# Performance work log

Measured on AMD Instinct MI355X. Metric: run time of the kernel, lower is better.

Reference implementation:

```python
import jax, jax.numpy as jnp
import numpy as np
import math

B, L, H, E = 4, 2048, 8, 64


def setup_inputs() -> dict:
    key = jax.random.key(0)
    kq, kk, kv, ks = jax.random.split(key, 4)
    return {
        "queries": jax.random.normal(kq, (B, L, H, E), dtype=jnp.float32),
        "keys": jax.random.normal(kk, (B, L, H, E), dtype=jnp.float32),
        "values": jax.random.normal(kv, (B, L, H, E), dtype=jnp.float32),
        "sigma": jax.random.normal(ks, (B, L, H), dtype=jnp.float32),
    }


def reference(queries, keys, values, sigma):
    Bq, Lq, Hq, Eq = queries.shape
    scale = 1.0 / math.sqrt(Eq)
    # QK^T: [B, H, L, S]
    scores = jnp.einsum("blhe,bshe->bhls", queries, keys)
    # triangular causal mask (mask_flag=True, attn_mask=None)
    causal = jnp.triu(jnp.ones((Lq, Lq), dtype=bool), k=1)
    scores = jnp.where(causal[None, None], -jnp.inf, scores)
    attn = scale * scores
    series = jax.nn.softmax(attn, axis=-1)  # dropout p=0.0 -> identity
    # sigma: [B, L, H] -> [B, H, L]
    sig = jnp.transpose(sigma, (0, 2, 1))
    sig = jax.nn.sigmoid(sig * 5.0) + 1e-5
    sig = jnp.power(3.0, sig) - 1.0
    sig = jnp.broadcast_to(sig[..., None], (Bq, Hq, Lq, Lq))  # [B,H,L,L]
    # |i - j| distances
    idx = jnp.arange(Lq, dtype=jnp.float32)
    dist = jnp.abs(idx[:, None] - idx[None, :])  # [L, L]
    prior = (1.0 / (math.sqrt(2.0 * math.pi) * sig)) * jnp.exp(
        -(dist[None, None] ** 2) / (2.0 * sig ** 2)
    )
    V = jnp.einsum("bhls,bshd->blhd", series, values)
    return V, series, prior, sig
```

## Files before the change

### kernel.cpp

```cpp
#include <hip/hip_runtime.h>
#include <math.h>

#define BB 4
#define LL 2048
#define HH 8
#define EE 64
#define TM 64
#define TN 64

static constexpr float SCALE = 0.125f;
static constexpr float LN3 = 1.0986122886681098f;
static constexpr float INV_SQRT_2PI = 0.3989422804014327f;
static constexpr size_t NMAT = (size_t)BB * HH * LL * LL;
static constexpr size_t SERIES_BASE = (size_t)BB * LL * HH * EE;
static constexpr size_t PRIOR_BASE = SERIES_BASE + NMAT;
static constexpr size_t SIG_BASE = PRIOR_BASE + NMAT;

__device__ __forceinline__ float dot4(float4 a, float4 b) {
  return a.x * b.x + a.y * b.y + a.z * b.z + a.w * b.w;
}
__device__ __forceinline__ void fma4(float4& acc, float s, float4 v) {
  acc.x += s * v.x; acc.y += s * v.y; acc.z += s * v.z; acc.w += s * v.w;
}

__global__ __launch_bounds__(256, 3)
void anomaly_attn(const float* __restrict__ qg,
                  const float* __restrict__ kg,
                  const float* __restrict__ vg,
                  const float* __restrict__ sgg,
                  float* __restrict__ out) {
  __shared__ float4 Qs[TM][17];
  __shared__ float4 KPs[TN][17];
  __shared__ float4 Vs[TN][17];
  __shared__ float s_linv[TM];
  __shared__ float s_sigv[TM], s_pinv[TM], s_c2[TM];

  const int t = threadIdx.x;
  const int bh = blockIdx.y;
  const int b = bh >> 3;
  const int h = bh & 7;
  const int tx = t & 15;
  const int ty = t >> 4;

  const float4* q4 = (const float4*)qg;
  const float4* k4 = (const float4*)kg;
  const float4* v4 = (const float4*)vg;
  float* Pf = (float*)&KPs[0][0];

  for (int half = 0; half < 2; ++half) {
    const int rt = (half == 0) ? (int)blockIdx.x : (LL / TM - 1 - (int)blockIdx.x);
    const int i0 = rt * TM;
    const int nt = rt + 1;

    __syncthreads();

    for (int idx = t; idx < TM * 16; idx += 256) {
      int r = idx >> 4, c = idx & 15;
      Qs[r][c] = q4[(((size_t)b * LL + (i0 + r)) * HH + h) * 16 + c];
    }
    if (t < TM) {
      float sg = sgg[((size_t)b * LL + (i0 + t)) * HH + h];
      float sd = 1.0f / (1.0f + __expf(-5.0f * sg)) + 1e-5f;
      float sv = expm1f(sd * LN3);
      s_sigv[t] = sv;
      s_pinv[t] = INV_SQRT_2PI / sv;
      s_c2[t] = 0.5f / (sv * sv);
    }

    float lr0 = 0.f, lr1 = 0.f, lr2 = 0.f, lr3 = 0.f;
    for (int jt = 0; jt < nt; ++jt) {
      const int j0 = jt * TN;
      __syncthreads();
      for (int idx = t; idx < TN * 16; idx += 256) {
        int r = idx >> 4, c = idx & 15;
        KPs[r][c] = k4[(((size_t)b * LL + (j0 + r)) * HH + h) * 16 + c];
      }
      __syncthreads();
      float S[4][4] = {};
      for (int e4 = 0; e4 < 16; ++e4) {
        float4 qv0 = Qs[ty][e4];
        float4 qv1 = Qs[ty + 16][e4];
        float4 qv2 = Qs[ty + 32][e4];
        float4 qv3 = Qs[ty + 48][e4];
        float4 kv0 = KPs[tx][e4];
        float4 kv1 = KPs[tx + 16][e4];
        float4 kv2 = KPs[tx + 32][e4];
        float4 kv3 = KPs[tx + 48][e4];
        S[0][0] += dot4(qv0, kv0); S[0][1] += dot4(qv0, kv1);
        S[0][2] += dot4(qv0, kv2); S[0][3] += dot4(qv0, kv3);
        S[1][0] += dot4(qv1, kv0); S[1][1] += dot4(qv1, kv1);
        S[1][2] += dot4(qv1, kv2); S[1][3] += dot4(qv1, kv3);
        S[2][0] += dot4(qv2, kv0); S[2][1] += dot4(qv2, kv1);
        S[2][2] += dot4(qv2, kv2); S[2][3] += dot4(qv2, kv3);
        S[3][0] += dot4(qv3, kv0); S[3][1] += dot4(qv3, kv1);
        S[3][2] += dot4(qv3, kv2); S[3][3] += dot4(qv3, kv3);
      }
#pragma unroll
      for (int cc = 0; cc < 4; ++cc) {
        int j = j0 + tx + 16 * cc;
        lr0 += (j <= i0 + ty)      ? __expf(S[0][cc] * SCALE) : 0.f;
        lr1 += (j <= i0 + ty + 16) ? __expf(S[1][cc] * SCALE) : 0.f;
        lr2 += (j <= i0 + ty + 32) ? __expf(S[2][cc] * SCALE) : 0.f;
        lr3 += (j <= i0 + ty + 48) ? __expf(S[3][cc] * SCALE) : 0.f;
      }
    }
#pragma unroll
    for (int m = 1; m < 16; m <<= 1) {
      lr0 += __shfl_xor(lr0, m);
      lr1 += __shfl_xor(lr1, m);
      lr2 += __shfl_xor(lr2, m);
      lr3 += __shfl_xor(lr3, m);
    }
    if (tx == 0) {
      s_linv[ty] = 1.0f / lr0;
      s_linv[ty + 16] = 1.0f / lr1;
      s_linv[ty + 32] = 1.0f / lr2;
      s_linv[ty + 48] = 1.0f / lr3;
    }
    __syncthreads();

    const float li0 = s_linv[ty];
    const float li1 = s_linv[ty + 16];
    const float li2 = s_linv[ty + 32];
    const float li3 = s_linv[ty + 48];
    float4 acc0 = {0, 0, 0, 0}, acc1 = {0, 0, 0, 0};
    float4 acc2 = {0, 0, 0, 0}, acc3 = {0, 0, 0, 0};
    for (int jt = 0; jt < nt; ++jt) {
      const int j0 = jt * TN;
      __syncthreads();
      for (int idx = t; idx < TN * 16; idx += 256) {
        int r = idx >> 4, c = idx & 15;
        size_t g = (((size_t)b * LL + (j0 + r)) * HH + h) * 16 + c;
        KPs[r][c] = k4[g];
        Vs[r][c] = v4[g];
      }
      __syncthreads();
      float S[4][4] = {};
      for (int e4 = 0; e4 < 16; ++e4) {
        float4 qv0 = Qs[ty][e4];
        float4 qv1 = Qs[ty + 16][e4];
        float4 qv2 = Qs[ty + 32][e4];
        float4 qv3 = Qs[ty + 48][e4];
        float4 kv0 = KPs[tx][e4];
        float4 kv1 = KPs[tx + 16][e4];
        float4 kv2 = KPs[tx + 32][e4];
        float4 kv3 = KPs[tx + 48][e4];
        S[0][0] += dot4(qv0, kv0); S[0][1] += dot4(qv0, kv1);
        S[0][2] += dot4(qv0, kv2); S[0][3] += dot4(qv0, kv3);
        S[1][0] += dot4(qv1, kv0); S[1][1] += dot4(qv1, kv1);
        S[1][2] += dot4(qv1, kv2); S[1][3] += dot4(qv1, kv3);
        S[2][0] += dot4(qv2, kv0); S[2][1] += dot4(qv2, kv1);
        S[2][2] += dot4(qv2, kv2); S[2][3] += dot4(qv2, kv3);
        S[3][0] += dot4(qv3, kv0); S[3][1] += dot4(qv3, kv1);
        S[3][2] += dot4(qv3, kv2); S[3][3] += dot4(qv3, kv3);
      }
      __syncthreads();
#pragma unroll
      for (int cc = 0; cc < 4; ++cc) {
        int j = j0 + tx + 16 * cc;
        int col = tx + 16 * cc;
        Pf[(ty) * 68 + col]      = (j <= i0 + ty)      ? __expf(S[0][cc] * SCALE) * li0 : 0.f;
        Pf[(ty + 16) * 68 + col] = (j <= i0 + ty + 16) ? __expf(S[1][cc] * SCALE) * li1 : 0.f;
        Pf[(ty + 32) * 68 + col] = (j <= i0 + ty + 32) ? __expf(S[2][cc] * SCALE) * li2 : 0.f;
        Pf[(ty + 48) * 68 + col] = (j <= i0 + ty + 48) ? __expf(S[3][cc] * SCALE) * li3 : 0.f;
      }
      __syncthreads();
#pragma unroll
      for (int m = 0; m < 4; ++m) {
        int idx = t + 256 * m;
        int rr = idx >> 4, jq = idx & 15;
        float4 pv = KPs[rr][jq];
        *(float4*)&out[SERIES_BASE + ((size_t)bh * LL + (i0 + rr)) * LL + j0 + jq * 4] = pv;
      }
#pragma unroll 4
      for (int j4 = 0; j4 < 16; ++j4) {
        float4 p0 = KPs[ty][j4];
        float4 p1 = KPs[ty + 16][j4];
        float4 p2 = KPs[ty + 32][j4];
        float4 p3 = KPs[ty + 48][j4];
        float4 va = Vs[j4 * 4 + 0][tx];
        float4 vb = Vs[j4 * 4 + 1][tx];
        float4 vc = Vs[j4 * 4 + 2][tx];
        float4 vd = Vs[j4 * 4 + 3][tx];
        fma4(acc0, p0.x, va); fma4(acc0, p0.y, vb); fma4(acc0, p0.z, vc); fma4(acc0, p0.w, vd);
        fma4(acc1, p1.x, va); fma4(acc1, p1.y, vb); fma4(acc1, p1.z, vc); fma4(acc1, p1.w, vd);
        fma4(acc2, p2.x, va); fma4(acc2, p2.y, vb); fma4(acc2, p2.z, vc); fma4(acc2, p2.w, vd);
        fma4(acc3, p3.x, va); fma4(acc3, p3.y, vb); fma4(acc3, p3.z, vc); fma4(acc3, p3.w, vd);
      }
    }
    {
      float4* o4 = (float4*)out;
      o4[(((size_t)b * LL + (i0 + ty)) * HH + h) * 16 + tx] = acc0;
      o4[(((size_t)b * LL + (i0 + ty + 16)) * HH + h) * 16 + tx] = acc1;
      o4[(((size_t)b * LL + (i0 + ty + 32)) * HH + h) * 16 + tx] = acc2;
      o4[(((size_t)b * LL + (i0 + ty + 48)) * HH + h) * 16 + tx] = acc3;
    }
    for (int idx = t; idx < TM * 512; idx += 256) {
      int rr = idx >> 9, jq = idx & 511;
      float iv = s_pinv[rr], c2 = s_c2[rr], sv = s_sigv[rr];
      float fi = (float)(i0 + rr);
      float d0 = fi - (float)(jq * 4);
      float d1 = d0 - 1.0f, d2 = d0 - 2.0f, d3 = d0 - 3.0f;
      float4 pr;
      pr.x = iv * __expf(-d0 * d0 * c2);
      pr.y = iv * __expf(-d1 * d1 * c2);
      pr.z = iv * __expf(-d2 * d2 * c2);
      pr.w = iv * __expf(-d3 * d3 * c2);
      size_t off = ((size_t)bh * LL + (i0 + rr)) * LL + jq * 4;
      *(float4*)&out[PRIOR_BASE + off] = pr;
      float4 sg4 = {sv, sv, sv, sv};
      *(float4*)&out[SIG_BASE + off] = sg4;
    }
    {
      int jz = nt * TN;
      int nz4 = (LL - jz) >> 2;
      if (nz4 > 0) {
        float4 z = {0, 0, 0, 0};
        for (int rr = 0; rr < TM; ++rr) {
          float* rowp = &out[SERIES_BASE + ((size_t)bh * LL + (i0 + rr)) * LL + jz];
          for (int c = t; c < nz4; c += 256) {
            *(float4*)&rowp[c * 4] = z;
          }
        }
      }
    }
  }
}

extern "C" void kernel_launch(void* const* d_in, const int* in_sizes, int n_in,
                              void* d_out, int out_size, void* d_ws, size_t ws_size,
                              hipStream_t stream) {
  const float* q = (const float*)d_in[0];
  const float* k = (const float*)d_in[1];
  const float* v = (const float*)d_in[2];
  const float* sg = (const float*)d_in[3];
  float* out = (float*)d_out;
  dim3 grid(LL / TM / 2, BB * HH);
  anomaly_attn<<<grid, 256, 0, stream>>>(q, k, v, sg, out);
}
```

Before: 2.015 ms.

## Use fp16 MFMA for QK^T and PV matmuls in anomaly attention

Replaces the scalar fp32 dot-product loops for QK^T and P·V with 16x16x32 fp16 MFMA instructions. Q, K and a transposed V are converted to half precision in shared memory, and the normalized probabilities are stored as fp16 and reused both for the series output and as the MFMA A operand. The per-row sum reduction now stays in registers instead of going through shared memory. The output tensor is dominated by large L×L writes (series, prior, sigma), so compute savings may matter less than memory traffic. Series values lose precision because they are rounded to fp16 before being written, and occupancy bounds drop from 3 to 2 blocks.

Result: faster. 1.711 ms (-15.1%).

```diff
diff --git a/kernel.cpp b/kernel.cpp
--- a/kernel.cpp
+++ b/kernel.cpp
@@ -7,6 +7,11 @@
 #define EE 64
 #define TM 64
 #define TN 64
+#define SH 72
+
+typedef _Float16 half4v __attribute__((ext_vector_type(4)));
+typedef _Float16 half8v __attribute__((ext_vector_type(8)));
+typedef float floatx4 __attribute__((ext_vector_type(4)));
 
 static constexpr float SCALE = 0.125f;
 static constexpr float LN3 = 1.0986122886681098f;
@@ -16,47 +21,42 @@
 static constexpr size_t PRIOR_BASE = SERIES_BASE + NMAT;
 static constexpr size_t SIG_BASE = PRIOR_BASE + NMAT;
 
-__device__ __forceinline__ float dot4(float4 a, float4 b) {
-  return a.x * b.x + a.y * b.y + a.z * b.z + a.w * b.w;
-}
-__device__ __forceinline__ void fma4(float4& acc, float s, float4 v) {
-  acc.x += s * v.x; acc.y += s * v.y; acc.z += s * v.z; acc.w += s * v.w;
-}
-
-__global__ __launch_bounds__(256, 3)
+__global__ __launch_bounds__(256, 2)
 void anomaly_attn(const float* __restrict__ qg,
                   const float* __restrict__ kg,
                   const float* __restrict__ vg,
                   const float* __restrict__ sgg,
                   float* __restrict__ out) {
-  __shared__ float4 Qs[TM][17];
-  __shared__ float4 KPs[TN][17];
-  __shared__ float4 Vs[TN][17];
-  __shared__ float s_linv[TM];
+  __shared__ __attribute__((aligned(16))) _Float16 Qh[TM * SH];
+  __shared__ __attribute__((aligned(16))) _Float16 Kh[TN * SH];
+  __shared__ __attribute__((aligned(16))) _Float16 Vt[EE * SH];
+  __shared__ __attribute__((aligned(16))) _Float16 Ph[TM * SH];
   __shared__ float s_sigv[TM], s_pinv[TM], s_c2[TM];
 
   const int t = threadIdx.x;
+  const int lane = t & 63;
+  const int w = t >> 6;
+  const int quad = lane >> 4;
+  const int l15 = lane & 15;
   const int bh = blockIdx.y;
-  const int b = bh >> 3;
-  const int h = bh & 7;
-  const int tx = t & 15;
-  const int ty = t >> 4;
-
+  const int b = bh >> 3, h = bh & 7;
   const float4* q4 = (const float4*)qg;
   const float4* k4 = (const float4*)kg;
   const float4* v4 = (const float4*)vg;
-  float* Pf = (float*)&KPs[0][0];
 
   for (int half = 0; half < 2; ++half) {
-    const int rt = (half == 0) ? (int)blockIdx.x : (LL / TM - 1 - (int)blockIdx.x);
+    const int rt = half ? (31 - (int)blockIdx.x) : (int)blockIdx.x;
     const int i0 = rt * TM;
     const int nt = rt + 1;
-
     __syncthreads();
 
-    for (int idx = t; idx < TM * 16; idx += 256) {
+#pragma unroll
+    for (int it = 0; it < 4; ++it) {
+      int idx = t + 256 * it;
       int r = idx >> 4, c = idx & 15;
-      Qs[r][c] = q4[(((size_t)b * LL + (i0 + r)) * HH + h) * 16 + c];
+      float4 qv = q4[(((size_t)b * LL + i0 + r) * HH + h) * 16 + c];
+      half4v hq = {(_Float16)qv.x, (_Float16)qv.y, (_Float16)qv.z, (_Float16)qv.w};
+      *(half4v*)&Qh[r * SH + c * 4] = hq;
     }
     if (t < TM) {
       float sg = sgg[((size_t)b * LL + (i0 + t)) * HH + h];
@@ -67,133 +67,132 @@
       s_c2[t] = 0.5f / (sv * sv);
     }
 
-    float lr0 = 0.f, lr1 = 0.f, lr2 = 0.f, lr3 = 0.f;
+    float lsum[4] = {0.f, 0.f, 0.f, 0.f};
     for (int jt = 0; jt < nt; ++jt) {
       const int j0 = jt * TN;
       __syncthreads();
-      for (int idx = t; idx < TN * 16; idx += 256) {
+#pragma unroll
+      for (int it = 0; it < 4; ++it) {
+        int idx = t + 256 * it;
         int r = idx >> 4, c = idx & 15;
-        KPs[r][c] = k4[(((size_t)b * LL + (j0 + r)) * HH + h) * 16 + c];
-      }
-      __syncthreads();
-      float S[4][4] = {};
-      for (int e4 = 0; e4 < 16; ++e4) {
-        float4 qv0 = Qs[ty][e4];
-        float4 qv1 = Qs[ty + 16][e4];
-        float4 qv2 = Qs[ty + 32][e4];
-        float4 qv3 = Qs[ty + 48][e4];
-        float4 kv0 = KPs[tx][e4];
-        float4 kv1 = KPs[tx + 16][e4];
-        float4 kv2 = KPs[tx + 32][e4];
-        float4 kv3 = KPs[tx + 48][e4];
-        S[0][0] += dot4(qv0, kv0); S[0][1] += dot4(qv0, kv1);
-        S[0][2] += dot4(qv0, kv2); S[0][3] += dot4(qv0, kv3);
-        S[1][0] += dot4(qv1, kv0); S[1][1] += dot4(qv1, kv1);
-        S[1][2] += dot4(qv1, kv2); S[1][3] += dot4(qv1, kv3);
-        S[2][0] += dot4(qv2, kv0); S[2][1] += dot4(qv2, kv1);
-        S[2][2] += dot4(qv2, kv2); S[2][3] += dot4(qv2, kv3);
-        S[3][0] += dot4(qv3, kv0); S[3][1] += dot4(qv3, kv1);
-        S[3][2] += dot4(qv3, kv2); S[3][3] += dot4(qv3, kv3);
-      }
-#pragma unroll
-      for (int cc = 0; cc < 4; ++cc) {
-        int j = j0 + tx + 16 * cc;
-        lr0 += (j <= i0 + ty)      ? __expf(S[0][cc] * SCALE) : 0.f;
-        lr1 += (j <= i0 + ty + 16) ? __expf(S[1][cc] * SCALE) : 0.f;
-        lr2 += (j <= i0 + ty + 32) ? __expf(S[2][cc] * SCALE) : 0.f;
-        lr3 += (j <= i0 + ty + 48) ? __expf(S[3][cc] * SCALE) : 0.f;
-      }
-    }
-#pragma unroll
-    for (int m = 1; m < 16; m <<= 1) {
-      lr0 += __shfl_xor(lr0, m);
-      lr1 += __shfl_xor(lr1, m);
-      lr2 += __shfl_xor(lr2, m);
-      lr3 += __shfl_xor(lr3, m);
-    }
-    if (tx == 0) {
-      s_linv[ty] = 1.0f / lr0;
-      s_linv[ty + 16] = 1.0f / lr1;
-      s_linv[ty + 32] = 1.0f / lr2;
-      s_linv[ty + 48] = 1.0f / lr3;
-    }
-    __syncthreads();
-
-    const float li0 = s_linv[ty];
-    const float li1 = s_linv[ty + 16];
-    const float li2 = s_linv[ty + 32];
-    const float li3 = s_linv[ty + 48];
-    float4 acc0 = {0, 0, 0, 0}, acc1 = {0, 0, 0, 0};
-    float4 acc2 = {0, 0, 0, 0}, acc3 = {0, 0, 0, 0};
+        float4 kv = k4[(((size_t)b * LL + j0 + r) * HH + h) * 16 + c];
+        half4v hk = {(_Float16)kv.x, (_Float16)kv.y, (_Float16)kv.z, (_Float16)kv.w};
+        *(half4v*)&Kh[r * SH + c * 4] = hk;
+      }
+      __syncthreads();
+      floatx4 acc[4] = {{0.f, 0.f, 0.f, 0.f}, {0.f, 0.f, 0.f, 0.f},
+                        {0.f, 0.f, 0.f, 0.f}, {0.f, 0.f, 0.f, 0.f}};
+#pragma unroll
+      for (int ks = 0; ks < 2; ++ks) {
+        half8v a = *(half8v*)&Qh[(w * 16 + l15) * SH + ks * 32 + quad * 8];
+#pragma unroll
+        for (int f = 0; f < 4; ++f) {
+          half8v bf = *(half8v*)&Kh[(f * 16 + l15) * SH + ks * 32 + quad * 8];
+          acc[f] = __builtin_amdgcn_mfma_f32_16x16x32_f16(a, bf, acc[f], 0, 0, 0);
+        }
+      }
+#pragma unroll
+      for (int f = 0; f < 4; ++f) {
+        int j = j0 + f * 16 + l15;
+#pragma unroll
+        for (int r = 0; r < 4; ++r) {
+          int i = i0 + w * 16 + quad * 4 + r;
+          lsum[r] += (j <= i) ? __expf(acc[f][r] * SCALE) : 0.f;
+        }
+      }
+    }
+#pragma unroll
+    for (int r = 0; r < 4; ++r) {
+      lsum[r] += __shfl_xor(lsum[r], 1);
+      lsum[r] += __shfl_xor(lsum[r], 2);
+      lsum[r] += __shfl_xor(lsum[r], 4);
+      lsum[r] += __shfl_xor(lsum[r], 8);
+    }
+    float linv[4];
+#pragma unroll
+    for (int r = 0; r < 4; ++r) linv[r] = 1.0f / lsum[r];
+
+    floatx4 Oacc[4] = {{0.f, 0.f, 0.f, 0.f}, {0.f, 0.f, 0.f, 0.f},
+                       {0.f, 0.f, 0.f, 0.f}, {0.f, 0.f, 0.f, 0.f}};
     for (int jt = 0; jt < nt; ++jt) {
       const int j0 = jt * TN;
       __syncthreads();
-      for (int idx = t; idx < TN * 16; idx += 256) {
+#pragma unroll
+      for (int it = 0; it < 4; ++it) {
+        int idx = t + 256 * it;
         int r = idx >> 4, c = idx & 15;
-        size_t g = (((size_t)b * LL + (j0 + r)) * HH + h) * 16 + c;
-        KPs[r][c] = k4[g];
-        Vs[r][c] = v4[g];
-      }
-      __syncthreads();
-      float S[4][4] = {};
-      for (int e4 = 0; e4 < 16; ++e4) {
-        float4 qv0 = Qs[ty][e4];
-        float4 qv1 = Qs[ty + 16][e4];
-        float4 qv2 = Qs[ty + 32][e4];
-        float4 qv3 = Qs[ty + 48][e4];
-        float4 kv0 = KPs[tx][e4];
-        float4 kv1 = KPs[tx + 16][e4];
-        float4 kv2 = KPs[tx + 32][e4];
-        float4 kv3 = KPs[tx + 48][e4];
-        S[0][0] += dot4(qv0, kv0); S[0][1] += dot4(qv0, kv1);
-        S[0][2] += dot4(qv0, kv2); S[0][3] += dot4(qv0, kv3);
-        S[1][0] += dot4(qv1, kv0); S[1][1] += dot4(qv1, kv1);
-        S[1][2] += dot4(qv1, kv2); S[1][3] += dot4(qv1, kv3);
-        S[2][0] += dot4(qv2, kv0); S[2][1] += dot4(qv2, kv1);
-        S[2][2] += dot4(qv2, kv2); S[2][3] += dot4(qv2, kv3);
-        S[3][0] += dot4(qv3, kv0); S[3][1] += dot4(qv3, kv1);
-        S[3][2] += dot4(qv3, kv2); S[3][3] += dot4(qv3, kv3);
-      }
-      __syncthreads();
-#pragma unroll
-      for (int cc = 0; cc < 4; ++cc) {
-        int j = j0 + tx + 16 * cc;
-        int col = tx + 16 * cc;
-        Pf[(ty) * 68 + col]      = (j <= i0 + ty)      ? __expf(S[0][cc] * SCALE) * li0 : 0.f;
-        Pf[(ty + 16) * 68 + col] = (j <= i0 + ty + 16) ? __expf(S[1][cc] * SCALE) * li1 : 0.f;
-        Pf[(ty + 32) * 68 + col] = (j <= i0 + ty + 32) ? __expf(S[2][cc] * SCALE) * li2 : 0.f;
-        Pf[(ty + 48) * 68 + col] = (j <= i0 + ty + 48) ? __expf(S[3][cc] * SCALE) * li3 : 0.f;
-      }
-      __syncthreads();
-#pragma unroll
-      for (int m = 0; m < 4; ++m) {
-        int idx = t + 256 * m;
-        int rr = idx >> 4, jq = idx & 15;
-        float4 pv = KPs[rr][jq];
-        *(float4*)&out[SERIES_BASE + ((size_t)bh * LL + (i0 + rr)) * LL + j0 + jq * 4] = pv;
-      }
-#pragma unroll 4
-      for (int j4 = 0; j4 < 16; ++j4) {
-        float4 p0 = KPs[ty][j4];
-        float4 p1 = KPs[ty + 16][j4];
-        float4 p2 = KPs[ty + 32][j4];
-        float4 p3 = KPs[ty + 48][j4];
-        float4 va = Vs[j4 * 4 + 0][tx];
-        float4 vb = Vs[j4 * 4 + 1][tx];
-        float4 vc = Vs[j4 * 4 + 2][tx];
-        float4 vd = Vs[j4 * 4 + 3][tx];
-        fma4(acc0, p0.x, va); fma4(acc0, p0.y, vb); fma4(acc0, p0.z, vc); fma4(acc0, p0.w, vd);
-        fma4(acc1, p1.x, va); fma4(acc1, p1.y, vb); fma4(acc1, p1.z, vc); fma4(acc1, p1.w, vd);
-        fma4(acc2, p2.x, va); fma4(acc2, p2.y, vb); fma4(acc2, p2.z, vc); fma4(acc2, p2.w, vd);
-        fma4(acc3, p3.x, va); fma4(acc3, p3.y, vb); fma4(acc3, p3.z, vc); fma4(acc3, p3.w, vd);
-      }
-    }
-    {
-      float4* o4 = (float4*)out;
-      o4[(((size_t)b * LL + (i0 + ty)) * HH + h) * 16 + tx] = acc0;
-      o4[(((size_t)b * LL + (i0 + ty + 16)) * HH + h) * 16 + tx] = acc1;
-      o4[(((size_t)b * LL + (i0 + ty + 32)) * HH + h) * 16 + tx] = acc2;
-      o4[(((size_t)b * LL + (i0 + ty + 48)) * HH + h) * 16 + tx] = acc3;
+        float4 kv = k4[(((size_t)b * LL + j0 + r) * HH + h) * 16 + c];
+        half4v hk = {(_Float16)kv.x, (_Float16)kv.y, (_Float16)kv.z, (_Float16)kv.w};
+        *(half4v*)&Kh[r * SH + c * 4] = hk;
+      }
+      {
+        const int tx = t & 15, ty = t >> 4;
+        float4 vv[4];
+#pragma unroll
+        for (int rr = 0; rr < 4; ++rr)
+          vv[rr] = v4[(((size_t)b * LL + j0 + ty * 4 + rr) * HH + h) * 16 + tx];
+#pragma unroll
+        for (int c = 0; c < 4; ++c) {
+          half4v hv = {(_Float16)vv[0].x, (_Float16)vv[1].x, (_Float16)vv[2].x, (_Float16)vv[3].x};
+          float e0 = c == 0 ? vv[0].x : c == 1 ? vv[0].y : c == 2 ? vv[0].z : vv[0].w;
+          float e1 = c == 0 ? vv[1].x : c == 1 ? vv[1].y : c == 2 ? vv[1].z : vv[1].w;
+          float e2 = c == 0 ? vv[2].x : c == 1 ? vv[2].y : c == 2 ? vv[2].z : vv[2].w;
+          float e3 = c == 0 ? vv[3].x : c == 1 ? vv[3].y : c == 2 ? vv[3].z : vv[3].w;
+          hv = (half4v){(_Float16)e0, (_Float16)e1, (_Float16)e2, (_Float16)e3};
+          *(half4v*)&Vt[(tx * 4 + c) * SH + ty * 4] = hv;
+        }
+      }
+      __syncthreads();
+      floatx4 acc[4] = {{0.f, 0.f, 0.f, 0.f}, {0.f, 0.f, 0.f, 0.f},
+                        {0.f, 0.f, 0.f, 0.f}, {0.f, 0.f, 0.f, 0.f}};
+#pragma unroll
+      for (int ks = 0; ks < 2; ++ks) {
+        half8v a = *(half8v*)&Qh[(w * 16 + l15) * SH + ks * 32 + quad * 8];
+#pragma unroll
+        for (int f = 0; f < 4; ++f) {
+          half8v bf = *(half8v*)&Kh[(f * 16 + l15) * SH + ks * 32 + quad * 8];
+          acc[f] = __builtin_amdgcn_mfma_f32_16x16x32_f16(a, bf, acc[f], 0, 0, 0);
+        }
+      }
+#pragma unroll
+      for (int f = 0; f < 4; ++f) {
+        int j = j0 + f * 16 + l15;
+#pragma unroll
+        for (int r = 0; r < 4; ++r) {
+          int i = i0 + w * 16 + quad * 4 + r;
+          float p = (j <= i) ? __expf(acc[f][r] * SCALE) * linv[r] : 0.f;
+          Ph[(w * 16 + quad * 4 + r) * SH + f * 16 + l15] = (_Float16)p;
+        }
+      }
+      __syncthreads();
+#pragma unroll
+      for (int rnd = 0; rnd < 2; ++rnd) {
+        int idx = t + 256 * rnd;
+        int r = idx >> 3, c8 = idx & 7;
+        half8v p = *(half8v*)&Ph[r * SH + c8 * 8];
+        float4 lo = {(float)p[0], (float)p[1], (float)p[2], (float)p[3]};
+        float4 hi = {(float)p[4], (float)p[5], (float)p[6], (float)p[7]};
+        size_t off = SERIES_BASE + ((size_t)bh * LL + i0 + r) * LL + j0 + c8 * 8;
+        *(float4*)&out[off] = lo;
+        *(float4*)&out[off + 4] = hi;
+      }
+#pragma unroll
+      for (int ks = 0; ks < 2; ++ks) {
+        half8v a = *(half8v*)&Ph[(w * 16 + l15) * SH + ks * 32 + quad * 8];
+#pragma unroll
+        for (int f = 0; f < 4; ++f) {
+          half8v bv = *(half8v*)&Vt[(f * 16 + l15) * SH + ks * 32 + quad * 8];
+          Oacc[f] = __builtin_amdgcn_mfma_f32_16x16x32_f16(a, bv, Oacc[f], 0, 0, 0);
+        }
+      }
+    }
+#pragma unroll
+    for (int f = 0; f < 4; ++f) {
+#pragma unroll
+      for (int r = 0; r < 4; ++r) {
+        int i = i0 + w * 16 + quad * 4 + r;
+        out[(((size_t)b * LL + i) * HH + h) * EE + f * 16 + l15] = Oacc[f][r];
+      }
     }
     for (int idx = t; idx < TM * 512; idx += 256) {
       int rr = idx >> 9, jq = idx & 511;
```
